# Kernel optimization log

Hardware: AMD Instinct MI355X
Metric: run time of the kernel (lower is better)

The kernel has to match this reference:

```python
import jax, jax.numpy as jnp
import numpy as np

B, T, S, D = 32, 128, 2048, 1024


def setup_inputs() -> dict:
    key = jax.random.key(0)
    k1, k2, k3, k4 = jax.random.split(key, 4)
    source = jax.random.normal(k1, (B, T, D), dtype=jnp.float32)
    memory_bank = jax.random.normal(k2, (B, S, D), dtype=jnp.float32)
    # lengths in [1, S] so no query row is fully masked
    memory_lengths = jax.random.randint(k3, (B,), 1, S + 1, dtype=jnp.int64)
    # nn.Linear(2*dim, dim, bias=False) weight, torch layout [out, in]
    bound = 1.0 / np.sqrt(2 * D)
    W_out = jax.random.uniform(k4, (D, 2 * D), dtype=jnp.float32, minval=-bound, maxval=bound)
    return {"source": source, "memory_bank": memory_bank,
            "W_out": W_out, "memory_lengths": memory_lengths}


def reference(source, memory_bank, W_out, memory_lengths):
    # dot score: [B, T, S]
    align = jnp.einsum("btd,bsd->bts", source, memory_bank)
    # sequence mask from lengths: [B, S]
    mask = jnp.arange(S)[None, :] < memory_lengths[:, None]
    align = jnp.where(mask[:, None, :], align, -jnp.inf)
    align_vectors = jax.nn.softmax(align, axis=-1)            # [B, T, S]
    c = jnp.einsum("bts,bsd->btd", align_vectors, memory_bank)  # [B, T, D]
    concat_c = jnp.concatenate([c, source], axis=-1)            # [B, T, 2D]
    attn_h = jnp.tanh(concat_c @ W_out.T)                       # [B, T, D]
    # transpose to [T, B, ...] as original (one_step=False path)
    return attn_h.transpose(1, 0, 2), align_vectors.transpose(1, 0, 2)
```

## Files before the change

### kernel.cpp

```cpp
#include <hip/hip_runtime.h>
#include <hip/hip_bf16.h>
#include <stdint.h>

#define B_ 32
#define T_ 128
#define S_ 2048
#define D_ 1024

typedef float floatx4 __attribute__((ext_vector_type(4)));
typedef float f32x4 __attribute__((ext_vector_type(4)));
typedef unsigned short u16x4 __attribute__((ext_vector_type(4)));
typedef unsigned short u16x8 __attribute__((ext_vector_type(8)));
typedef __bf16 bf16x8 __attribute__((ext_vector_type(8)));

__device__ __forceinline__ unsigned short f2bf(float x){
  __hip_bfloat16 h = __float2bfloat16(x);
  return __builtin_bit_cast(unsigned short, h);
}
__device__ __forceinline__ float bf2f(unsigned short u){
  __hip_bfloat16 h = __builtin_bit_cast(__hip_bfloat16, u);
  return __bfloat162float(h);
}
__device__ __forceinline__ f32x4 mfma16(u16x8 a, u16x8 b, f32x4 c){
  return __builtin_amdgcn_mfma_f32_16x16x32_bf16(
      __builtin_bit_cast(bf16x8, a), __builtin_bit_cast(bf16x8, b), c, 0, 0, 0);
}

__global__ __launch_bounds__(512, 4) void k_align(
    const float* __restrict__ src, const float* __restrict__ mb,
    float* __restrict__ logits)
{
  __shared__ unsigned short Ah[128][40], Al[128][40], Bh[128][40], Bl[128][40];
  const int b = blockIdx.x, sblk = blockIdx.y;
  const int tid = threadIdx.x, lane = tid & 63, wave = tid >> 6;
  const int wr = wave >> 2, wc = wave & 3;
  const float* Ag = src + (size_t)b * T_ * D_;
  const float* Bg = mb + (size_t)b * S_ * D_ + (size_t)sblk * 128 * D_;

  f32x4 acc[4][2];
  #pragma unroll
  for (int m = 0; m < 4; m++)
    #pragma unroll
    for (int n = 0; n < 2; n++) acc[m][n] = (f32x4){0.f, 0.f, 0.f, 0.f};

  floatx4 ra[2], rb[2];
  #pragma unroll
  for (int j = 0; j < 2; j++) {
    int f4 = tid + 512 * j;
    int row = f4 >> 3, c4 = (f4 & 7) * 4;
    ra[j] = *(const floatx4*)(Ag + (size_t)row * D_ + c4);
    rb[j] = *(const floatx4*)(Bg + (size_t)row * D_ + c4);
  }

  for (int k0 = 0; k0 < D_; k0 += 32) {
    #pragma unroll
    for (int j = 0; j < 2; j++) {
      int f4 = tid + 512 * j;
      int row = f4 >> 3, c4 = (f4 & 7) * 4;
      u16x4 ah, al, bh, bl;
      #pragma unroll
      for (int i = 0; i < 4; i++) {
        unsigned short h = f2bf(ra[j][i]); float hf = bf2f(h);
        ah[i] = h; al[i] = f2bf(ra[j][i] - hf);
        h = f2bf(rb[j][i]); hf = bf2f(h);
        bh[i] = h; bl[i] = f2bf(rb[j][i] - hf);
      }
      *(u16x4*)&Ah[row][c4] = ah;
      *(u16x4*)&Al[row][c4] = al;
      *(u16x4*)&Bh[row][c4] = bh;
      *(u16x4*)&Bl[row][c4] = bl;
    }
    __syncthreads();
    if (k0 + 32 < D_) {
      #pragma unroll
      for (int j = 0; j < 2; j++) {
        int f4 = tid + 512 * j;
        int row = f4 >> 3, c4 = (f4 & 7) * 4;
        ra[j] = *(const floatx4*)(Ag + (size_t)row * D_ + (k0 + 32) + c4);
        rb[j] = *(const floatx4*)(Bg + (size_t)row * D_ + (k0 + 32) + c4);
      }
    }
    {
      const int kb = (lane >> 4) << 3;
      u16x8 a_h[4], a_l[4], b_h[2], b_l[2];
      #pragma unroll
      for (int m = 0; m < 4; m++) {
        int r = wr * 64 + m * 16 + (lane & 15);
        a_h[m] = *(const u16x8*)&Ah[r][kb];
        a_l[m] = *(const u16x8*)&Al[r][kb];
      }
      #pragma unroll
      for (int n = 0; n < 2; n++) {
        int r = wc * 32 + n * 16 + (lane & 15);
        b_h[n] = *(const u16x8*)&Bh[r][kb];
        b_l[n] = *(const u16x8*)&Bl[r][kb];
      }
      #pragma unroll
      for (int m = 0; m < 4; m++)
        #pragma unroll
        for (int n = 0; n < 2; n++) {
          acc[m][n] = mfma16(a_h[m], b_h[n], acc[m][n]);
          acc[m][n] = mfma16(a_h[m], b_l[n], acc[m][n]);
          acc[m][n] = mfma16(a_l[m], b_h[n], acc[m][n]);
        }
    }
    __syncthreads();
  }
  #pragma unroll
  for (int m = 0; m < 4; m++)
    #pragma unroll
    for (int n = 0; n < 2; n++)
      #pragma unroll
      for (int j = 0; j < 4; j++) {
        int t = wr * 64 + m * 16 + ((lane >> 4) << 2) + j;
        int s = sblk * 128 + wc * 32 + n * 16 + (lane & 15);
        logits[((size_t)b * T_ + t) * S_ + s] = acc[m][n][j];
      }
}

__global__ __launch_bounds__(256) void k_softmax(
    float* __restrict__ logits, const int* __restrict__ lens,
    float* __restrict__ out1)
{
  const int bt = blockIdx.x;
  const int b = bt >> 7, t = bt & 127;
  const int probe = lens[1];
  const int len = (probe == 0) ? lens[2 * b] : lens[b];
  float* row = logits + (size_t)bt * S_;
  const int tid = threadIdx.x, lane = tid & 63, wave = tid >> 6;

  floatx4 v[2];
  float mx = -3.0e38f;
  #pragma unroll
  for (int j = 0; j < 2; j++) {
    int f4 = tid + 256 * j;
    v[j] = *(const floatx4*)(row + f4 * 4);
    #pragma unroll
    for (int i = 0; i < 4; i++) {
      int s = f4 * 4 + i;
      if (s < len) mx = fmaxf(mx, v[j][i]);
    }
  }
  #pragma unroll
  for (int off = 1; off < 64; off <<= 1) mx = fmaxf(mx, __shfl_xor(mx, off));
  __shared__ float red[8];
  if (lane == 0) red[wave] = mx;
  __syncthreads();
  mx = fmaxf(fmaxf(red[0], red[1]), fmaxf(red[2], red[3]));

  float sum = 0.f;
  floatx4 e[2];
  #pragma unroll
  for (int j = 0; j < 2; j++) {
    int f4 = tid + 256 * j;
    #pragma unroll
    for (int i = 0; i < 4; i++) {
      int s = f4 * 4 + i;
      float ee = (s < len) ? __expf(v[j][i] - mx) : 0.f;
      e[j][i] = ee; sum += ee;
    }
  }
  #pragma unroll
  for (int off = 1; off < 64; off <<= 1) sum += __shfl_xor(sum, off);
  if (lane == 0) red[4 + wave] = sum;
  __syncthreads();
  sum = red[4] + red[5] + red[6] + red[7];
  const float inv = 1.0f / sum;

  float* orow = out1 + ((size_t)t * B_ + b) * S_;
  #pragma unroll
  for (int j = 0; j < 2; j++) {
    int f4 = tid + 256 * j;
    floatx4 o;
    #pragma unroll
    for (int i = 0; i < 4; i++) o[i] = e[j][i] * inv;
    *(floatx4*)(row + f4 * 4) = o;
    *(floatx4*)(orow + f4 * 4) = o;
  }
}

__global__ __launch_bounds__(512, 2) void k_pv(
    const float* __restrict__ p, const float* __restrict__ mb,
    float* __restrict__ cout)
{
  __shared__ unsigned short As[128][72];
  __shared__ unsigned short BsT[128][72];
  const int b = blockIdx.x, dblk = blockIdx.y;
  const int tid = threadIdx.x, lane = tid & 63, wave = tid >> 6;
  const int wr = wave >> 2, wc = wave & 3;
  const float* Pg = p + (size_t)b * T_ * S_;
  const float* Bg = mb + (size_t)b * S_ * D_ + dblk * 128;

  f32x4 acc[4][2];
  #pragma unroll
  for (int m = 0; m < 4; m++)
    #pragma unroll
    for (int n = 0; n < 2; n++) acc[m][n] = (f32x4){0.f, 0.f, 0.f, 0.f};

  const int gs = tid & 15, gd = tid >> 4;
  const int s0 = gs * 4, d0 = gd * 4;

  floatx4 ra[4], rb[4];
  #pragma unroll
  for (int j = 0; j < 4; j++) {
    int f4 = tid + 512 * j;
    int row = f4 >> 4, c4 = (f4 & 15) * 4;
    ra[j] = *(const floatx4*)(Pg + (size_t)row * S_ + c4);
    rb[j] = *(const floatx4*)(Bg + (size_t)(s0 + j) * D_ + d0);
  }

  for (int k0 = 0; k0 < S_; k0 += 64) {
    #pragma unroll
    for (int j = 0; j < 4; j++) {
      int f4 = tid + 512 * j;
      int row = f4 >> 4, c4 = (f4 & 15) * 4;
      u16x4 ah;
      #pragma unroll
      for (int i = 0; i < 4; i++) ah[i] = f2bf(ra[j][i]);
      *(u16x4*)&As[row][c4] = ah;
    }
    #pragma unroll
    for (int jj = 0; jj < 4; jj++) {
      u16x4 w = { f2bf(rb[0][jj]), f2bf(rb[1][jj]), f2bf(rb[2][jj]), f2bf(rb[3][jj]) };
      *(u16x4*)&BsT[d0 + jj][s0] = w;
    }
    __syncthreads();
    if (k0 + 64 < S_) {
      #pragma unroll
      for (int j = 0; j < 4; j++) {
        int f4 = tid + 512 * j;
        int row = f4 >> 4, c4 = (f4 & 15) * 4;
        ra[j] = *(const floatx4*)(Pg + (size_t)row * S_ + (k0 + 64) + c4);
        rb[j] = *(const floatx4*)(Bg + (size_t)(k0 + 64 + s0 + j) * D_ + d0);
      }
    }
    #pragma unroll
    for (int kk = 0; kk < 2; kk++) {
      int kb = kk * 32 + ((lane >> 4) << 3);
      u16x8 a[4], bb[2];
      #pragma unroll
      for (int m = 0; m < 4; m++)
        a[m] = *(const u16x8*)&As[wr * 64 + m * 16 + (lane & 15)][kb];
      #pragma unroll
      for (int n = 0; n < 2; n++)
        bb[n] = *(const u16x8*)&BsT[wc * 32 + n * 16 + (lane & 15)][kb];
      #pragma unroll
      for (int m = 0; m < 4; m++)
        #pragma unroll
        for (int n = 0; n < 2; n++)
          acc[m][n] = mfma16(a[m], bb[n], acc[m][n]);
    }
    __syncthreads();
  }
  #pragma unroll
  for (int m = 0; m < 4; m++)
    #pragma unroll
    for (int n = 0; n < 2; n++)
      #pragma unroll
      for (int j = 0; j < 4; j++) {
        int t = wr * 64 + m * 16 + ((lane >> 4) << 2) + j;
        int d = dblk * 128 + wc * 32 + n * 16 + (lane & 15);
        cout[((size_t)b * T_ + t) * D_ + d] = acc[m][n][j];
      }
}

__global__ __launch_bounds__(512, 2) void k_proj(
    const float* __restrict__ cbuf, const float* __restrict__ src,
    const float* __restrict__ w, float* __restrict__ out0)
{
  __shared__ unsigned short Ah[128][72], Bh[128][72];
  const int b = blockIdx.x, nblk = blockIdx.y;
  const int tid = threadIdx.x, lane = tid & 63, wave = tid >> 6;
  const int wr = wave >> 2, wc = wave & 3;
  const float* Ca = cbuf + (size_t)b * T_ * D_;
  const float* Sa = src + (size_t)b * T_ * D_;

  f32x4 acc[4][2];
  #pragma unroll
  for (int m = 0; m < 4; m++)
    #pragma unroll
    for (int n = 0; n < 2; n++) acc[m][n] = (f32x4){0.f, 0.f, 0.f, 0.f};

  floatx4 ra[4], rb[4];
  #pragma unroll
  for (int j = 0; j < 4; j++) {
    int f4 = tid + 512 * j;
    int row = f4 >> 4, c4 = (f4 & 15) * 4;
    ra[j] = *(const floatx4*)(Ca + (size_t)row * D_ + c4);
    rb[j] = *(const floatx4*)(w + (size_t)(nblk * 128 + row) * (2 * D_) + c4);
  }

  for (int k0 = 0; k0 < 2 * D_; k0 += 64) {
    #pragma unroll
    for (int j = 0; j < 4; j++) {
      int f4 = tid + 512 * j;
      int row = f4 >> 4, c4 = (f4 & 15) * 4;
      u16x4 ah, bh;
      #pragma unroll
      for (int i = 0; i < 4; i++) { ah[i] = f2bf(ra[j][i]); bh[i] = f2bf(rb[j][i]); }
      *(u16x4*)&Ah[row][c4] = ah;
      *(u16x4*)&Bh[row][c4] = bh;
    }
    __syncthreads();
    if (k0 + 64 < 2 * D_) {
      int kn = k0 + 64;
      const float* Asrc = (kn < D_) ? (Ca + kn) : (Sa + (kn - D_));
      #pragma unroll
      for (int j = 0; j < 4; j++) {
        int f4 = tid + 512 * j;
        int row = f4 >> 4, c4 = (f4 & 15) * 4;
        ra[j] = *(const floatx4*)(Asrc + (size_t)row * D_ + c4);
        rb[j] = *(const floatx4*)(w + (size_t)(nblk * 128 + row) * (2 * D_) + kn + c4);
      }
    }
    #pragma unroll
    for (int kk = 0; kk < 2; kk++) {
      int kb = kk * 32 + ((lane >> 4) << 3);
      u16x8 a[4], bb[2];
      #pragma unroll
      for (int m = 0; m < 4; m++)
        a[m] = *(const u16x8*)&Ah[wr * 64 + m * 16 + (lane & 15)][kb];
      #pragma unroll
      for (int n = 0; n < 2; n++)
        bb[n] = *(const u16x8*)&Bh[wc * 32 + n * 16 + (lane & 15)][kb];
      #pragma unroll
      for (int m = 0; m < 4; m++)
        #pragma unroll
        for (int n = 0; n < 2; n++)
          acc[m][n] = mfma16(a[m], bb[n], acc[m][n]);
    }
    __syncthreads();
  }
  #pragma unroll
  for (int m = 0; m < 4; m++)
    #pragma unroll
    for (int n = 0; n < 2; n++)
      #pragma unroll
      for (int j = 0; j < 4; j++) {
        int t = wr * 64 + m * 16 + ((lane >> 4) << 2) + j;
        int d = nblk * 128 + wc * 32 + n * 16 + (lane & 15);
        out0[(size_t)t * (B_ * D_) + (size_t)b * D_ + d] = tanhf(acc[m][n][j]);
      }
}

extern "C" void kernel_launch(void* const* d_in, const int* in_sizes, int n_in,
                              void* d_out, int out_size, void* d_ws, size_t ws_size,
                              hipStream_t stream) {
  const float* src = (const float*)d_in[0];
  const float* mb  = (const float*)d_in[1];
  const float* w   = (const float*)d_in[2];
  const int*   len = (const int*)d_in[3];

  float* out0 = (float*)d_out;
  float* out1 = out0 + (size_t)T_ * B_ * D_;

  float* logits = (float*)d_ws;
  float* cbuf   = logits + (size_t)B_ * T_ * S_;

  k_align  <<<dim3(B_, S_ / 128), 512, 0, stream>>>(src, mb, logits);
  k_softmax<<<dim3(B_ * T_),      256, 0, stream>>>(logits, len, out1);
  k_pv     <<<dim3(B_, D_ / 128), 512, 0, stream>>>(logits, mb, cbuf);
  k_proj   <<<dim3(B_, D_ / 128), 512, 0, stream>>>(cbuf, src, w, out0);
}
```

Baseline: 220.2 us.

## Split PV GEMM along S into two partial sums reduced in projection

The P·V kernel grid gains a z dimension that splits the S reduction into two chunks, each writing a partial context buffer, so the grid doubles from 256 to 512 blocks and fills more compute units. The projection kernel now reads both partial buffers and adds them while converting to bf16, so no separate reduction kernel is needed. Launch bounds on k_pv are raised to 4 blocks per multiprocessor. The cost is an extra partial-buffer write and read plus extra workspace, and the code falls back to a single split if the workspace is too small.

```diff
diff --git a/kernel.cpp b/kernel.cpp
--- a/kernel.cpp
+++ b/kernel.cpp
@@ -179,17 +179,19 @@
   }
 }
 
-__global__ __launch_bounds__(512, 2) void k_pv(
+__global__ __launch_bounds__(512, 4) void k_pv(
     const float* __restrict__ p, const float* __restrict__ mb,
-    float* __restrict__ cout)
+    float* __restrict__ cpart, int schunk)
 {
   __shared__ unsigned short As[128][72];
   __shared__ unsigned short BsT[128][72];
-  const int b = blockIdx.x, dblk = blockIdx.y;
+  const int b = blockIdx.x, dblk = blockIdx.y, z = blockIdx.z;
+  const int sbeg = z * schunk;
   const int tid = threadIdx.x, lane = tid & 63, wave = tid >> 6;
   const int wr = wave >> 2, wc = wave & 3;
   const float* Pg = p + (size_t)b * T_ * S_;
   const float* Bg = mb + (size_t)b * S_ * D_ + dblk * 128;
+  float* cout = cpart + (size_t)z * B_ * T_ * D_;
 
   f32x4 acc[4][2];
   #pragma unroll
@@ -205,11 +207,11 @@
   for (int j = 0; j < 4; j++) {
     int f4 = tid + 512 * j;
     int row = f4 >> 4, c4 = (f4 & 15) * 4;
-    ra[j] = *(const floatx4*)(Pg + (size_t)row * S_ + c4);
-    rb[j] = *(const floatx4*)(Bg + (size_t)(s0 + j) * D_ + d0);
-  }
-
-  for (int k0 = 0; k0 < S_; k0 += 64) {
+    ra[j] = *(const floatx4*)(Pg + (size_t)row * S_ + sbeg + c4);
+    rb[j] = *(const floatx4*)(Bg + (size_t)(sbeg + s0 + j) * D_ + d0);
+  }
+
+  for (int k0 = sbeg; k0 < sbeg + schunk; k0 += 64) {
     #pragma unroll
     for (int j = 0; j < 4; j++) {
       int f4 = tid + 512 * j;
@@ -225,7 +227,7 @@
       *(u16x4*)&BsT[d0 + jj][s0] = w;
     }
     __syncthreads();
-    if (k0 + 64 < S_) {
+    if (k0 + 64 < sbeg + schunk) {
       #pragma unroll
       for (int j = 0; j < 4; j++) {
         int f4 = tid + 512 * j;
@@ -265,14 +267,16 @@
 }
 
 __global__ __launch_bounds__(512, 2) void k_proj(
-    const float* __restrict__ cbuf, const float* __restrict__ src,
-    const float* __restrict__ w, float* __restrict__ out0)
+    const float* __restrict__ c0, const float* __restrict__ c1,
+    const float* __restrict__ src, const float* __restrict__ w,
+    float* __restrict__ out0, int two)
 {
   __shared__ unsigned short Ah[128][72], Bh[128][72];
   const int b = blockIdx.x, nblk = blockIdx.y;
   const int tid = threadIdx.x, lane = tid & 63, wave = tid >> 6;
   const int wr = wave >> 2, wc = wave & 3;
-  const float* Ca = cbuf + (size_t)b * T_ * D_;
+  const float* Ca = c0 + (size_t)b * T_ * D_;
+  const float* Cb = c1 + (size_t)b * T_ * D_;
   const float* Sa = src + (size_t)b * T_ * D_;
 
   f32x4 acc[4][2];
@@ -281,35 +285,45 @@
     #pragma unroll
     for (int n = 0; n < 2; n++) acc[m][n] = (f32x4){0.f, 0.f, 0.f, 0.f};
 
-  floatx4 ra[4], rb[4];
+  floatx4 ra[4], ra2[4], rb[4];
   #pragma unroll
   for (int j = 0; j < 4; j++) {
     int f4 = tid + 512 * j;
     int row = f4 >> 4, c4 = (f4 & 15) * 4;
-    ra[j] = *(const floatx4*)(Ca + (size_t)row * D_ + c4);
-    rb[j] = *(const floatx4*)(w + (size_t)(nblk * 128 + row) * (2 * D_) + c4);
+    ra[j]  = *(const floatx4*)(Ca + (size_t)row * D_ + c4);
+    ra2[j] = *(const floatx4*)(Cb + (size_t)row * D_ + c4);
+    rb[j]  = *(const floatx4*)(w + (size_t)(nblk * 128 + row) * (2 * D_) + c4);
   }
 
   for (int k0 = 0; k0 < 2 * D_; k0 += 64) {
+    const int in_c = (k0 < D_);
     #pragma unroll
     for (int j = 0; j < 4; j++) {
       int f4 = tid + 512 * j;
       int row = f4 >> 4, c4 = (f4 & 15) * 4;
       u16x4 ah, bh;
       #pragma unroll
-      for (int i = 0; i < 4; i++) { ah[i] = f2bf(ra[j][i]); bh[i] = f2bf(rb[j][i]); }
+      for (int i = 0; i < 4; i++) {
+        float av = ra[j][i];
+        if (in_c && two) av += ra2[j][i];
+        ah[i] = f2bf(av); bh[i] = f2bf(rb[j][i]);
+      }
       *(u16x4*)&Ah[row][c4] = ah;
       *(u16x4*)&Bh[row][c4] = bh;
     }
     __syncthreads();
     if (k0 + 64 < 2 * D_) {
       int kn = k0 + 64;
-      const float* Asrc = (kn < D_) ? (Ca + kn) : (Sa + (kn - D_));
       #pragma unroll
       for (int j = 0; j < 4; j++) {
         int f4 = tid + 512 * j;
         int row = f4 >> 4, c4 = (f4 & 15) * 4;
-        ra[j] = *(const floatx4*)(Asrc + (size_t)row * D_ + c4);
+        if (kn < D_) {
+          ra[j]  = *(const floatx4*)(Ca + (size_t)row * D_ + kn + c4);
+          ra2[j] = *(const floatx4*)(Cb + (size_t)row * D_ + kn + c4);
+        } else {
+          ra[j]  = *(const floatx4*)(Sa + (size_t)row * D_ + (kn - D_) + c4);
+        }
         rb[j] = *(const floatx4*)(w + (size_t)(nblk * 128 + row) * (2 * D_) + kn + c4);
       }
     }
@@ -355,10 +369,16 @@
   float* out1 = out0 + (size_t)T_ * B_ * D_;
 
   float* logits = (float*)d_ws;
-  float* cbuf   = logits + (size_t)B_ * T_ * S_;
+  float* c0 = logits + (size_t)B_ * T_ * S_;
+  float* c1 = c0 + (size_t)B_ * T_ * D_;
+
+  const size_t need2 = ((size_t)B_ * T_ * S_ + 2 * (size_t)B_ * T_ * D_) * 4;
+  const int nsplit = (ws_size >= need2) ? 2 : 1;
+  const int schunk = S_ / nsplit;
 
   k_align  <<<dim3(B_, S_ / 128), 512, 0, stream>>>(src, mb, logits);
   k_softmax<<<dim3(B_ * T_),      256, 0, stream>>>(logits, len, out1);
-  k_pv     <<<dim3(B_, D_ / 128), 512, 0, stream>>>(logits, mb, cbuf);
-  k_proj   <<<dim3(B_, D_ / 128), 512, 0, stream>>>(cbuf, src, w, out0);
-}
+  k_pv     <<<dim3(B_, D_ / 128, nsplit), 512, 0, stream>>>(logits, mb, c0, schunk);
+  k_proj   <<<dim3(B_, D_ / 128), 512, 0, stream>>>(c0, (nsplit == 2) ? c1 : c0,
+                                                    src, w, out0, nsplit == 2 ? 1 : 0);
+}
```

Measured after the change: 231.3 us. 5.0% more time.
